# Kernel tuning notes

Measured on AMD Instinct MI355X. Metric: run time of the kernel, lower is better.

Reference implementation:

```python
import jax, jax.numpy as jnp
import numpy as np

L = 128          # lifted_dim
NS = 50000       # source nodes
NT = 50000       # target nodes
E = 640000       # edges
SLOPE = 0.01     # cfg.leaky_slope (torch LeakyReLU default)
EPS = 1e-5       # BatchNorm eps


def _glorot(key, shape):
    fan_in, fan_out = shape[0], shape[1]
    lim = np.sqrt(6.0 / (fan_in + fan_out)).astype(np.float32)
    return jax.random.uniform(key, shape, jnp.float32, -lim, lim)


def setup_inputs() -> dict:
    key = jax.random.key(0)
    ks = jax.random.split(key, 16)
    x_s = jax.random.normal(ks[0], (NS, L), jnp.float32)
    x_t = jax.random.normal(ks[1], (NT, L), jnp.float32)
    edge_index = jax.random.randint(ks[2], (2, E), 0, NT, jnp.int64)
    edge_attr = jax.random.normal(ks[3], (E, L), jnp.float32)
    x_u = jax.random.normal(ks[4], (L,), jnp.float32)
    M = 2 * L  # message_dim
    U = 4 * L  # update_dim
    params = {
        'W1': _glorot(ks[5], (M, M)), 'b1': jnp.zeros((M,), jnp.float32),
        'W2': _glorot(ks[6], (M, M)), 'b2': jnp.zeros((M,), jnp.float32),
        'U1': _glorot(ks[7], (U, U)), 'c1': jnp.zeros((U,), jnp.float32),
        'U2': _glorot(ks[8], (U, L)), 'c2': jnp.zeros((L,), jnp.float32),
        'gamma': jnp.ones((L,), jnp.float32), 'beta': jnp.zeros((L,), jnp.float32),
    }
    return dict(x_s=x_s, x_t=x_t, edge_index=edge_index, edge_attr=edge_attr, x_u=x_u, **params)


def reference(x_s, x_t, edge_index, edge_attr, x_u,
              W1, b1, W2, b2, U1, c1, U2, c2, gamma, beta):
    src, tgt = edge_index[0], edge_index[1]
    # edge messages: gather source features + edge attrs -> 2-layer MLP
    msg = jnp.concatenate([x_s[src], edge_attr], axis=1)          # [E, 2L]
    msg = jax.nn.leaky_relu(msg @ W1 + b1, negative_slope=SLOPE)
    msg = msg @ W2 + b2                                           # [E, 2L]
    # scatter-add aggregation onto target nodes
    agg = jax.ops.segment_sum(msg, tgt, num_segments=x_t.shape[0])  # [NT, 2L]
    # node update
    xu = jnp.broadcast_to(x_u[None, :], (x_t.shape[0], x_u.shape[0]))
    h = jnp.concatenate([x_t, agg, xu], axis=-1)                  # [NT, 4L]
    h = jax.nn.leaky_relu(h @ U1 + c1, negative_slope=SLOPE)
    h = h @ U2 + c2                                               # [NT, L]
    # BatchNorm1d (training mode: batch statistics, biased variance)
    mu = jnp.mean(h, axis=0)
    var = jnp.var(h, axis=0)
    return gamma * (h - mu) * jax.lax.rsqrt(var + EPS) + beta
```

## Files before the change

kernel.cpp:

```cpp
#include <hip/hip_runtime.h>

typedef unsigned int u32;
typedef unsigned short u16;
typedef __attribute__((ext_vector_type(8))) short short8;
typedef __attribute__((ext_vector_type(8))) unsigned short ushort8v;
typedef __attribute__((ext_vector_type(4))) unsigned short ushort4v;
typedef __attribute__((ext_vector_type(4))) float f32x4;

#define NSRC 50000
#define NTGT 50000
#define NEDGE 640000
#define LDIM 128
#define SLOPE 0.01f

#define MFMA(a, b, c) __builtin_amdgcn_mfma_f32_16x16x32_bf16((a), (b), (c), 0, 0, 0)

__device__ __forceinline__ u16 f2bf(float f) {
  union { float f; u32 u; } v; v.f = f;
  u32 r = v.u + 0x7FFFu + ((v.u >> 16) & 1u);
  return (u16)(r >> 16);
}
__device__ __forceinline__ float bf2f(u16 h) {
  union { u32 u; float f; } v; v.u = ((u32)h) << 16; return v.f;
}

__global__ void k_w2b(const float* __restrict__ W2, const float* __restrict__ U1,
                      float* __restrict__ w2b) {
  const int i = blockIdx.x;
  const int j = threadIdx.x;
  const float* __restrict__ u = U1 + (size_t)128 * 512;
  float a0 = 0.f, a1 = 0.f;
#pragma unroll 8
  for (int k = 0; k < 256; ++k) {
    float w = W2[(size_t)i * 256 + k];
    a0 += w * u[(size_t)k * 512 + j];
    a1 += w * u[(size_t)k * 512 + j + 256];
  }
  w2b[(size_t)i * 512 + j] = a0;
  w2b[(size_t)i * 512 + j + 256] = a1;
}

__global__ void k_bias(const float* __restrict__ U1, const float* __restrict__ xu,
                       const float* __restrict__ b2, const float* __restrict__ c1,
                       float* __restrict__ c1e, float* __restrict__ vb) {
  const int j = threadIdx.x;
  float s = c1[j];
#pragma unroll 4
  for (int k = 0; k < 128; ++k) s += xu[k] * U1[(size_t)(384 + k) * 512 + j];
  float v = 0.f;
#pragma unroll 4
  for (int k = 0; k < 256; ++k) v += b2[k] * U1[(size_t)(128 + k) * 512 + j];
  c1e[j] = s;
  vb[j] = v;
}

__global__ void k_prep(const float* __restrict__ W1, const float* __restrict__ U1,
                       const float* __restrict__ U2, const float* __restrict__ w2b,
                       u16* __restrict__ w1a, u16* __restrict__ w1b,
                       u16* __restrict__ u1e, u16* __restrict__ u2p) {
  int id = blockIdx.x * 256 + threadIdx.x;
  int lane = id & 63, quad = (lane >> 4), l16 = lane & 15;
  if (id < 4096) {
    int g = id >> 6;
    int kc = g >> 4, cb = g & 15;
    const float* s = W1 + (size_t)(kc * 32 + quad * 8) * 256 + cb * 16 + l16;
    ushort8v p;
#pragma unroll
    for (int j = 0; j < 8; ++j) p[j] = f2bf(s[(size_t)j * 256]);
    *(ushort8v*)(w1a + ((size_t)g * 64 + lane) * 8) = p;
  } else if (id < 8192) {
    int g = (id - 4096) >> 6;
    int kc = g >> 4, cb = g & 15;
    const float* s = W1 + (size_t)(128 + kc * 32 + quad * 8) * 256 + cb * 16 + l16;
    ushort8v p;
#pragma unroll
    for (int j = 0; j < 8; ++j) p[j] = f2bf(s[(size_t)j * 256]);
    *(ushort8v*)(w1b + ((size_t)g * 64 + lane) * 8) = p;
  } else if (id < 32768) {
    int g = (id - 8192) >> 6;
    int kc = g >> 5, cb = g & 31;
    int col = cb * 16 + l16;
    ushort8v p;
#pragma unroll
    for (int j = 0; j < 8; ++j) {
      int row = kc * 32 + quad * 8 + j;
      float v = (row < 128) ? U1[(size_t)row * 512 + col]
                            : w2b[(size_t)(row - 128) * 512 + col];
      p[j] = f2bf(v);
    }
    *(ushort8v*)(u1e + ((size_t)g * 64 + lane) * 8) = p;
  } else if (id < 40960) {
    int g = (id - 32768) >> 6;
    int kc = g >> 3, cb = g & 7;
    const float* s = U2 + (size_t)(kc * 32 + quad * 8) * 128 + cb * 16 + l16;
    ushort8v p;
#pragma unroll
    for (int j = 0; j < 8; ++j) p[j] = f2bf(s[(size_t)j * 128]);
    *(ushort8v*)(u2p + ((size_t)g * 64 + lane) * 8) = p;
  }
}

__global__ void k_count(const int* __restrict__ tgt, int* __restrict__ cnt,
                        int* __restrict__ rank) {
  int e = blockIdx.x * 256 + threadIdx.x;
  if (e < NEDGE) rank[e] = atomicAdd(&cnt[tgt[e]], 1);
}

__global__ void k_scan(const int* __restrict__ cnt, int* __restrict__ rowstart) {
  __shared__ int part[1024];
  int tid = threadIdx.x;
  int base = tid * 49;
  int s = 0;
  for (int i = 0; i < 49; ++i) { int idx = base + i; if (idx < NTGT) s += cnt[idx]; }
  part[tid] = s;
  __syncthreads();
  for (int off = 1; off < 1024; off <<= 1) {
    int v = (tid >= off) ? part[tid - off] : 0;
    __syncthreads();
    part[tid] += v;
    __syncthreads();
  }
  int run = (tid > 0) ? part[tid - 1] : 0;
  for (int i = 0; i < 49; ++i) {
    int idx = base + i;
    if (idx < NTGT) { rowstart[idx] = run; run += cnt[idx]; }
  }
  if (tid == 1023) rowstart[NTGT] = part[1023];
}

__global__ void k_posinv(const int* __restrict__ tgt, const int* __restrict__ rowstart,
                         const int* __restrict__ rank, int* __restrict__ order) {
  int e = blockIdx.x * 256 + threadIdx.x;
  if (e < NEDGE) order[rowstart[tgt[e]] + rank[e]] = e;
}

__global__ __launch_bounds__(256, 3) void k_pgemm(
    const float* __restrict__ xs, const u16* __restrict__ w1ap,
    const float* __restrict__ b1, u16* __restrict__ P) {
  __shared__ u16 At[64][136];
  __shared__ u16 Ot[64][264];
  const int tid = threadIdx.x;
  const int base = blockIdx.x * 64;
  {
    const int et = tid >> 2, p = tid & 3;
    const int row = base + et;
    u16* dst = &At[et][p * 32];
    if (row < NSRC) {
      const float4* f4 = (const float4*)(xs + (size_t)row * LDIM + p * 32);
#pragma unroll
      for (int i = 0; i < 4; ++i) {
        float4 a = f4[2 * i], b = f4[2 * i + 1];
        ushort8v pk = { f2bf(a.x), f2bf(a.y), f2bf(a.z), f2bf(a.w),
                        f2bf(b.x), f2bf(b.y), f2bf(b.z), f2bf(b.w) };
        *(ushort8v*)(dst + i * 8) = pk;
      }
    } else {
      ushort8v z = {0, 0, 0, 0, 0, 0, 0, 0};
#pragma unroll
      for (int i = 0; i < 4; ++i) *(ushort8v*)(dst + i * 8) = z;
    }
  }
  __syncthreads();

  const int lane = tid & 63, wid = tid >> 6;
  const int quad = lane >> 4, l16 = lane & 15;
  const int colb = wid * 64;
  const short8* __restrict__ wf = (const short8*)w1ap;

  f32x4 acc[4][4];
#pragma unroll
  for (int a = 0; a < 4; ++a)
#pragma unroll
    for (int b = 0; b < 4; ++b) acc[a][b] = (f32x4){0.f, 0.f, 0.f, 0.f};
#pragma unroll
  for (int kc = 0; kc < 4; ++kc) {
    short8 af[4], bfr[4];
#pragma unroll
    for (int ct = 0; ct < 4; ++ct)
      bfr[ct] = wf[(size_t)(kc * 16 + wid * 4 + ct) * 64 + lane];
#pragma unroll
    for (int rt = 0; rt < 4; ++rt)
      af[rt] = *(const short8*)&At[rt * 16 + l16][kc * 32 + quad * 8];
#pragma unroll
    for (int rt = 0; rt < 4; ++rt)
#pragma unroll
      for (int ct = 0; ct < 4; ++ct)
        acc[rt][ct] = MFMA(af[rt], bfr[ct], acc[rt][ct]);
  }
#pragma unroll
  for (int ct = 0; ct < 4; ++ct) {
    int col = colb + ct * 16 + l16;
    float bias = b1[col];
#pragma unroll
    for (int rt = 0; rt < 4; ++rt)
#pragma unroll
      for (int r = 0; r < 4; ++r) {
        int row = rt * 16 + quad * 4 + r;
        Ot[row][col] = f2bf(acc[rt][ct][r] + bias);
      }
  }
  __syncthreads();
  {
    const int et = tid >> 2, p = tid & 3;
    const int row = base + et;
    if (row < NSRC) {
      u16* dst = P + (size_t)row * 256 + p * 64;
      const u16* sl = &Ot[et][p * 64];
#pragma unroll
      for (int i = 0; i < 8; ++i)
        *(ushort8v*)(dst + i * 8) = *(const ushort8v*)(sl + i * 8);
    }
  }
}

__global__ __launch_bounds__(256, 4) void k_edge(
    const float* __restrict__ ea, const int* __restrict__ srcp,
    const int* __restrict__ tgtp, const int* __restrict__ order,
    const u16* __restrict__ Pg, const u16* __restrict__ w1bp,
    float* __restrict__ agg) {
  __shared__ u16 Pt[64][264];
  __shared__ int s_tgt[64];
  __shared__ unsigned long long s_mask;
  const int tid = threadIdx.x;
  const int base = blockIdx.x * 64;

  {
    const int et = tid >> 2, p = tid & 3;
    const int e = order[base + et];
    if (p == 0) s_tgt[et] = tgtp[e];
    const int sidx = srcp[e];
    const ushort8v* pr = (const ushort8v*)(Pg + (size_t)sidx * 256 + p * 64);
    u16* dst = &Pt[et][p * 64];
#pragma unroll
    for (int i = 0; i < 8; ++i) *(ushort8v*)(dst + i * 8) = pr[i];
  }
  if (tid < 64) {
    int tcur = tgtp[order[base + tid]];
    int tprv = (tid > 0) ? tgtp[order[base + tid - 1]] : tcur;
    unsigned long long m = __ballot(tcur != tprv);
    if (tid == 0) s_mask = m;
  }

  const int lane = tid & 63, wid = tid >> 6;
  const int quad = lane >> 4, l16 = lane & 15;
  const short8* __restrict__ wf = (const short8*)w1bp;

  const int myrow = wid * 16 + l16;
  const float* arow = ea + (size_t)order[base + myrow] * LDIM + quad * 8;

  short8 af[4];
#pragma unroll
  for (int kc = 0; kc < 4; ++kc) {
    f32x4 x = *(const f32x4*)(arow + kc * 32);
    f32x4 y = *(const f32x4*)(arow + kc * 32 + 4);
    af[kc] = (short8){ (short)f2bf(x[0]), (short)f2bf(x[1]),
                       (short)f2bf(x[2]), (short)f2bf(x[3]),
                       (short)f2bf(y[0]), (short)f2bf(y[1]),
                       (short)f2bf(y[2]), (short)f2bf(y[3]) };
  }

  f32x4 acc[8];
#pragma unroll
  for (int ct = 0; ct < 8; ++ct) acc[ct] = (f32x4){0.f, 0.f, 0.f, 0.f};
#pragma unroll
  for (int kc = 0; kc < 4; ++kc)
#pragma unroll
    for (int ct = 0; ct < 8; ++ct)
      acc[ct] = MFMA(af[kc], wf[(size_t)(kc * 16 + ct) * 64 + lane], acc[ct]);

  __syncthreads();

#pragma unroll
  for (int ct = 0; ct < 8; ++ct) {
    int col = ct * 16 + l16;
#pragma unroll
    for (int r = 0; r < 4; ++r) {
      int row = wid * 16 + quad * 4 + r;
      float v = acc[ct][r] + bf2f(Pt[row][col]);
      v = v > 0.f ? v : SLOPE * v;
      Pt[row][col] = f2bf(v);
    }
  }

#pragma unroll
  for (int ct = 0; ct < 8; ++ct) acc[ct] = (f32x4){0.f, 0.f, 0.f, 0.f};
#pragma unroll
  for (int kc = 0; kc < 4; ++kc)
#pragma unroll
    for (int ct = 0; ct < 8; ++ct)
      acc[ct] = MFMA(af[kc], wf[(size_t)(kc * 16 + 8 + ct) * 64 + lane], acc[ct]);

#pragma unroll
  for (int ct = 0; ct < 8; ++ct) {
    int col = 128 + ct * 16 + l16;
#pragma unroll
    for (int r = 0; r < 4; ++r) {
      int row = wid * 16 + quad * 4 + r;
      float v = acc[ct][r] + bf2f(Pt[row][col]);
      v = v > 0.f ? v : SLOPE * v;
      Pt[row][col] = f2bf(v);
    }
  }
  __syncthreads();

  {
    const unsigned long long mask = s_mask;
    const int col = tid;
    float accv = 0.f;
    int segstart = 0;
    for (int r = 0; r < 64; ++r) {
      if ((mask >> r) & 1ull) {
        float* dst = agg + (size_t)s_tgt[r - 1] * 256 + col;
        if (segstart == 0) atomicAdd(dst, accv);
        else *dst = accv;
        accv = 0.f; segstart = r;
      }
      accv += bf2f(Pt[r][col]);
    }
    atomicAdd(agg + (size_t)s_tgt[63] * 256 + col, accv);
  }
}

__global__ __launch_bounds__(256, 4) void k_node(
    const float* __restrict__ xt, const float* __restrict__ agg,
    const int* __restrict__ rowstart, const u16* __restrict__ u1e,
    const u16* __restrict__ u2p, const float* __restrict__ c1e,
    const float* __restrict__ vb, const float* __restrict__ c2,
    float* __restrict__ h2, float* __restrict__ stats) {
  __shared__ u16 ain[32][520];
  __shared__ float sdeg[32];
  const int tid = threadIdx.x;
  const int lane = tid & 63, wid = tid >> 6;
  const int quad = lane >> 4, l16 = lane & 15;
  const int tbase = blockIdx.x * 32;

  for (int s = wid; s < 32; s += 4) {
    int t = tbase + s;
    if (t < NTGT) {
      if (lane < 32) {
        float4 v = ((const float4*)(xt + (size_t)t * LDIM))[lane];
        ushort4v p = { f2bf(v.x), f2bf(v.y), f2bf(v.z), f2bf(v.w) };
        *(ushort4v*)&ain[s][lane * 4] = p;
      }
      if (lane == 0) sdeg[s] = (float)(rowstart[t + 1] - rowstart[t]);
      float4 v = ((const float4*)(agg + (size_t)t * 256))[lane];
      ushort4v p = { f2bf(v.x), f2bf(v.y), f2bf(v.z), f2bf(v.w) };
      *(ushort4v*)&ain[s][128 + lane * 4] = p;
    } else {
      ushort8v z = {0, 0, 0, 0, 0, 0, 0, 0};
      *(ushort8v*)&ain[s][lane * 8] = z;
      if (lane == 0) sdeg[s] = 0.f;
    }
  }
  __syncthreads();

  const short8* __restrict__ u1f = (const short8*)u1e;
  const short8* __restrict__ u2f = (const short8*)u2p;

  f32x4 acc[2][2][4];
#pragma unroll
  for (int h = 0; h < 2; ++h)
#pragma unroll
    for (int a = 0; a < 2; ++a)
#pragma unroll
      for (int b = 0; b < 4; ++b) acc[h][a][b] = (f32x4){0.f, 0.f, 0.f, 0.f};

#pragma unroll 2
  for (int kc = 0; kc < 12; ++kc) {
    short8 af[2];
#pragma unroll
    for (int rt = 0; rt < 2; ++rt)
      af[rt] = *(const short8*)&ain[rt * 16 + l16][kc * 32 + quad * 8];
#pragma unroll
    for (int h = 0; h < 2; ++h) {
      short8 bfr[4];
#pragma unroll
      for (int ct = 0; ct < 4; ++ct)
        bfr[ct] = u1f[(size_t)(kc * 32 + h * 16 + wid * 4 + ct) * 64 + lane];
#pragma unroll
      for (int rt = 0; rt < 2; ++rt)
#pragma unroll
        for (int ct = 0; ct < 4; ++ct)
          acc[h][rt][ct] = MFMA(af[rt], bfr[ct], acc[h][rt][ct]);
    }
  }
  __syncthreads();
#pragma unroll
  for (int h = 0; h < 2; ++h)
#pragma unroll
    for (int ct = 0; ct < 4; ++ct) {
      int col = h * 256 + wid * 64 + ct * 16 + l16;
      float cb = c1e[col], vbb = vb[col];
#pragma unroll
      for (int rt = 0; rt < 2; ++rt)
#pragma unroll
        for (int r = 0; r < 4; ++r) {
          int row = rt * 16 + quad * 4 + r;
          float v = acc[h][rt][ct][r] + cb + sdeg[row] * vbb;
          v = v > 0.f ? v : SLOPE * v;
          ain[row][col] = f2bf(v);
        }
    }
  __syncthreads();

  const int colb2 = wid * 32;
  f32x4 acc2[2][2];
#pragma unroll
  for (int a = 0; a < 2; ++a)
#pragma unroll
    for (int b = 0; b < 2; ++b) acc2[a][b] = (f32x4){0.f, 0.f, 0.f, 0.f};
#pragma unroll 4
  for (int kc = 0; kc < 16; ++kc) {
    short8 af[2], bfr[2];
#pragma unroll
    for (int ct = 0; ct < 2; ++ct)
      bfr[ct] = u2f[(size_t)(kc * 8 + wid * 2 + ct) * 64 + lane];
#pragma unroll
    for (int rt = 0; rt < 2; ++rt)
      af[rt] = *(const short8*)&ain[rt * 16 + l16][kc * 32 + quad * 8];
#pragma unroll
    for (int rt = 0; rt < 2; ++rt)
#pragma unroll
      for (int ct = 0; ct < 2; ++ct)
        acc2[rt][ct] = MFMA(af[rt], bfr[ct], acc2[rt][ct]);
  }
  float s1[2] = {0.f, 0.f}, s2[2] = {0.f, 0.f};
#pragma unroll
  for (int ct = 0; ct < 2; ++ct) {
    int col = colb2 + ct * 16 + l16;
    float cb = c2[col];
#pragma unroll
    for (int rt = 0; rt < 2; ++rt)
#pragma unroll
      for (int r = 0; r < 4; ++r) {
        int row = rt * 16 + quad * 4 + r;
        int t = tbase + row;
        if (t < NTGT) {
          float v = acc2[rt][ct][r] + cb;
          h2[(size_t)t * LDIM + col] = v;
          s1[ct] += v; s2[ct] += v * v;
        }
      }
  }
#pragma unroll
  for (int ct = 0; ct < 2; ++ct) {
    float a = s1[ct], b = s2[ct];
    a += __shfl_down(a, 32); b += __shfl_down(b, 32);
    a += __shfl_down(a, 16); b += __shfl_down(b, 16);
    if (lane < 16) {
      atomicAdd(&stats[colb2 + ct * 16 + l16], a);
      atomicAdd(&stats[128 + colb2 + ct * 16 + l16], b);
    }
  }
}

__global__ void k_bnfin(const float* __restrict__ stats, const float* __restrict__ gamma,
                        const float* __restrict__ beta, float* __restrict__ ss) {
  int c = threadIdx.x;
  if (c < 128) {
    float mu = stats[c] * (1.0f / NTGT);
    float var = stats[128 + c] * (1.0f / NTGT) - mu * mu;
    float rs = rsqrtf(var + 1e-5f);
    float sc = gamma[c] * rs;
    ss[c] = sc;
    ss[128 + c] = beta[c] - mu * sc;
  }
}

__global__ void k_bnapply(const float* __restrict__ h2, const float* __restrict__ ss,
                          float* __restrict__ out) {
  int i = blockIdx.x * 256 + threadIdx.x;
  const int total = NTGT * LDIM / 4;
  const float4* h4 = (const float4*)h2;
  const float4* sc4 = (const float4*)ss;
  const float4* sh4 = (const float4*)(ss + 128);
  float4* o4 = (float4*)out;
  for (; i < total; i += gridDim.x * 256) {
    int cg = i & 31;
    float4 h = h4[i], sc = sc4[cg], sh = sh4[cg];
    float4 r = { h.x * sc.x + sh.x, h.y * sc.y + sh.y,
                 h.z * sc.z + sh.z, h.w * sc.w + sh.w };
    o4[i] = r;
  }
}

extern "C" void kernel_launch(void* const* d_in, const int* in_sizes, int n_in,
                              void* d_out, int out_size, void* d_ws, size_t ws_size,
                              hipStream_t stream) {
  (void)in_sizes; (void)n_in; (void)out_size; (void)ws_size;
  const float* xs    = (const float*)d_in[0];
  const float* xt    = (const float*)d_in[1];
  const int*   ei    = (const int*)d_in[2];
  const float* ea    = (const float*)d_in[3];
  const float* xu    = (const float*)d_in[4];
  const float* W1    = (const float*)d_in[5];
  const float* b1    = (const float*)d_in[6];
  const float* W2    = (const float*)d_in[7];
  const float* b2    = (const float*)d_in[8];
  const float* U1    = (const float*)d_in[9];
  const float* c1    = (const float*)d_in[10];
  const float* U2    = (const float*)d_in[11];
  const float* c2    = (const float*)d_in[12];
  const float* gamma = (const float*)d_in[13];
  const float* beta  = (const float*)d_in[14];

  char* ws = (char*)d_ws;
  u16* w1a   = (u16*)(ws + 0x000000);
  u16* w1b   = (u16*)(ws + 0x010000);
  u16* u1e   = (u16*)(ws + 0x020000);
  u16* u2p   = (u16*)(ws + 0x080000);
  float* w2b = (float*)(ws + 0x0A0000);
  float* c1e = (float*)(ws + 0x120000);
  float* vbv = (float*)(ws + 0x120800);
  int* cnt   = (int*)(ws + 0x130000);
  int* rowst = (int*)(ws + 0x161000);
  int* rank  = (int*)(ws + 0x192000);
  float* stats = (float*)(ws + 0x404000);
  float* ss    = stats + 256;
  int* order = (int*)(ws + 0x405000);
  float* agg = (float*)(ws + 0x680000);
  u16*   Pbuf = (u16*)(ws + 0x3760000);
  float* h2   = (float*)(ws + 0x3760000);

  const int* srcp = ei;
  const int* tgtp = ei + NEDGE;

  hipMemsetAsync(cnt, 0, NTGT * 4, stream);
  hipMemsetAsync(stats, 0, 256 * 4, stream);
  hipMemsetAsync(agg, 0, (size_t)NTGT * 256 * 4, stream);
  k_w2b<<<256, 256, 0, stream>>>(W2, U1, w2b);
  k_bias<<<1, 512, 0, stream>>>(U1, xu, b2, c1, c1e, vbv);
  k_prep<<<160, 256, 0, stream>>>(W1, U1, U2, w2b, w1a, w1b, u1e, u2p);
  k_count<<<2500, 256, 0, stream>>>(tgtp, cnt, rank);
  k_scan<<<1, 1024, 0, stream>>>(cnt, rowst);
  k_posinv<<<2500, 256, 0, stream>>>(tgtp, rowst, rank, order);
  k_pgemm<<<782, 256, 0, stream>>>(xs, w1a, b1, Pbuf);
  k_edge<<<10000, 256, 0, stream>>>(ea, srcp, tgtp, order, Pbuf, w1b, agg);
  k_node<<<1563, 256, 0, stream>>>(xt, agg, rowst, u1e, u2p, c1e, vbv, c2, h2, stats);
  k_bnfin<<<1, 128, 0, stream>>>(stats, gamma, beta, ss);
  k_bnapply<<<6250, 256, 0, stream>>>(h2, ss, (float*)d_out);
}
```

Before: 948.6 us.

## Process two edge tiles per block and prefetch next tile's edge attributes

The edge kernel now handles two 64-edge tiles per block in a loop, halving the grid. While the first tile computes, it issues the global loads of edge_attr rows for the second tile into registers, hiding that load latency. The segmented reduction also batches 16 LDS reads at a time before the branchy accumulate loop. This costs extra registers for the prefetch buffer, which may reduce occupancy, and fewer blocks means less parallelism to hide latency.

```diff
diff --git a/kernel.cpp b/kernel.cpp
--- a/kernel.cpp
+++ b/kernel.cpp
@@ -222,102 +222,132 @@
   __shared__ int s_tgt[64];
   __shared__ unsigned long long s_mask;
   const int tid = threadIdx.x;
-  const int base = blockIdx.x * 64;
-
-  {
-    const int et = tid >> 2, p = tid & 3;
-    const int e = order[base + et];
-    if (p == 0) s_tgt[et] = tgtp[e];
-    const int sidx = srcp[e];
-    const ushort8v* pr = (const ushort8v*)(Pg + (size_t)sidx * 256 + p * 64);
-    u16* dst = &Pt[et][p * 64];
-#pragma unroll
-    for (int i = 0; i < 8; ++i) *(ushort8v*)(dst + i * 8) = pr[i];
-  }
-  if (tid < 64) {
-    int tcur = tgtp[order[base + tid]];
-    int tprv = (tid > 0) ? tgtp[order[base + tid - 1]] : tcur;
-    unsigned long long m = __ballot(tcur != tprv);
-    if (tid == 0) s_mask = m;
-  }
-
   const int lane = tid & 63, wid = tid >> 6;
   const int quad = lane >> 4, l16 = lane & 15;
+  const int myrow = wid * 16 + l16;
+  const int base0 = blockIdx.x * 128;
   const short8* __restrict__ wf = (const short8*)w1bp;
 
-  const int myrow = wid * 16 + l16;
-  const float* arow = ea + (size_t)order[base + myrow] * LDIM + quad * 8;
-
-  short8 af[4];
-#pragma unroll
-  for (int kc = 0; kc < 4; ++kc) {
-    f32x4 x = *(const f32x4*)(arow + kc * 32);
-    f32x4 y = *(const f32x4*)(arow + kc * 32 + 4);
-    af[kc] = (short8){ (short)f2bf(x[0]), (short)f2bf(x[1]),
-                       (short)f2bf(x[2]), (short)f2bf(x[3]),
-                       (short)f2bf(y[0]), (short)f2bf(y[1]),
-                       (short)f2bf(y[2]), (short)f2bf(y[3]) };
-  }
-
-  f32x4 acc[8];
-#pragma unroll
-  for (int ct = 0; ct < 8; ++ct) acc[ct] = (f32x4){0.f, 0.f, 0.f, 0.f};
-#pragma unroll
-  for (int kc = 0; kc < 4; ++kc)
-#pragma unroll
-    for (int ct = 0; ct < 8; ++ct)
-      acc[ct] = MFMA(af[kc], wf[(size_t)(kc * 16 + ct) * 64 + lane], acc[ct]);
-
-  __syncthreads();
-
-#pragma unroll
-  for (int ct = 0; ct < 8; ++ct) {
-    int col = ct * 16 + l16;
-#pragma unroll
-    for (int r = 0; r < 4; ++r) {
-      int row = wid * 16 + quad * 4 + r;
-      float v = acc[ct][r] + bf2f(Pt[row][col]);
-      v = v > 0.f ? v : SLOPE * v;
-      Pt[row][col] = f2bf(v);
-    }
-  }
-
-#pragma unroll
-  for (int ct = 0; ct < 8; ++ct) acc[ct] = (f32x4){0.f, 0.f, 0.f, 0.f};
-#pragma unroll
-  for (int kc = 0; kc < 4; ++kc)
-#pragma unroll
-    for (int ct = 0; ct < 8; ++ct)
-      acc[ct] = MFMA(af[kc], wf[(size_t)(kc * 16 + 8 + ct) * 64 + lane], acc[ct]);
-
-#pragma unroll
-  for (int ct = 0; ct < 8; ++ct) {
-    int col = 128 + ct * 16 + l16;
-#pragma unroll
-    for (int r = 0; r < 4; ++r) {
-      int row = wid * 16 + quad * 4 + r;
-      float v = acc[ct][r] + bf2f(Pt[row][col]);
-      v = v > 0.f ? v : SLOPE * v;
-      Pt[row][col] = f2bf(v);
-    }
-  }
-  __syncthreads();
-
+  const int em0 = order[base0 + myrow];
+  const int em1 = order[base0 + 64 + myrow];
+  f32x4 a0[8];
   {
-    const unsigned long long mask = s_mask;
-    const int col = tid;
-    float accv = 0.f;
-    int segstart = 0;
-    for (int r = 0; r < 64; ++r) {
-      if ((mask >> r) & 1ull) {
-        float* dst = agg + (size_t)s_tgt[r - 1] * 256 + col;
-        if (segstart == 0) atomicAdd(dst, accv);
-        else *dst = accv;
-        accv = 0.f; segstart = r;
-      }
-      accv += bf2f(Pt[r][col]);
-    }
-    atomicAdd(agg + (size_t)s_tgt[63] * 256 + col, accv);
+    const float* ar = ea + (size_t)em0 * LDIM + quad * 8;
+#pragma unroll
+    for (int kc = 0; kc < 4; ++kc) {
+      a0[2 * kc]     = *(const f32x4*)(ar + kc * 32);
+      a0[2 * kc + 1] = *(const f32x4*)(ar + kc * 32 + 4);
+    }
+  }
+
+#pragma unroll 1
+  for (int it = 0; it < 2; ++it) {
+    const int base = base0 + it * 64;
+
+    {
+      const int et = tid >> 2, p = tid & 3;
+      const int e = order[base + et];
+      if (p == 0) s_tgt[et] = tgtp[e];
+      const int sidx = srcp[e];
+      const ushort8v* pr = (const ushort8v*)(Pg + (size_t)sidx * 256 + p * 64);
+      u16* dst = &Pt[et][p * 64];
+#pragma unroll
+      for (int i = 0; i < 8; ++i) *(ushort8v*)(dst + i * 8) = pr[i];
+    }
+    if (tid < 64) {
+      int tcur = tgtp[order[base + tid]];
+      int tprv = (tid > 0) ? tgtp[order[base + tid - 1]] : tcur;
+      unsigned long long m = __ballot(tcur != tprv);
+      if (tid == 0) s_mask = m;
+    }
+
+    short8 af[4];
+#pragma unroll
+    for (int kc = 0; kc < 4; ++kc) {
+      f32x4 x = a0[2 * kc], y = a0[2 * kc + 1];
+      af[kc] = (short8){ (short)f2bf(x[0]), (short)f2bf(x[1]),
+                         (short)f2bf(x[2]), (short)f2bf(x[3]),
+                         (short)f2bf(y[0]), (short)f2bf(y[1]),
+                         (short)f2bf(y[2]), (short)f2bf(y[3]) };
+    }
+    if (it == 0) {
+      const float* ar = ea + (size_t)em1 * LDIM + quad * 8;
+#pragma unroll
+      for (int kc = 0; kc < 4; ++kc) {
+        a0[2 * kc]     = *(const f32x4*)(ar + kc * 32);
+        a0[2 * kc + 1] = *(const f32x4*)(ar + kc * 32 + 4);
+      }
+    }
+
+    f32x4 acc[8];
+#pragma unroll
+    for (int ct = 0; ct < 8; ++ct) acc[ct] = (f32x4){0.f, 0.f, 0.f, 0.f};
+#pragma unroll
+    for (int kc = 0; kc < 4; ++kc)
+#pragma unroll
+      for (int ct = 0; ct < 8; ++ct)
+        acc[ct] = MFMA(af[kc], wf[(size_t)(kc * 16 + ct) * 64 + lane], acc[ct]);
+
+    __syncthreads();
+
+#pragma unroll
+    for (int ct = 0; ct < 8; ++ct) {
+      int col = ct * 16 + l16;
+#pragma unroll
+      for (int r = 0; r < 4; ++r) {
+        int row = wid * 16 + quad * 4 + r;
+        float v = acc[ct][r] + bf2f(Pt[row][col]);
+        v = v > 0.f ? v : SLOPE * v;
+        Pt[row][col] = f2bf(v);
+      }
+    }
+
+#pragma unroll
+    for (int ct = 0; ct < 8; ++ct) acc[ct] = (f32x4){0.f, 0.f, 0.f, 0.f};
+#pragma unroll
+    for (int kc = 0; kc < 4; ++kc)
+#pragma unroll
+      for (int ct = 0; ct < 8; ++ct)
+        acc[ct] = MFMA(af[kc], wf[(size_t)(kc * 16 + 8 + ct) * 64 + lane], acc[ct]);
+
+#pragma unroll
+    for (int ct = 0; ct < 8; ++ct) {
+      int col = 128 + ct * 16 + l16;
+#pragma unroll
+      for (int r = 0; r < 4; ++r) {
+        int row = wid * 16 + quad * 4 + r;
+        float v = acc[ct][r] + bf2f(Pt[row][col]);
+        v = v > 0.f ? v : SLOPE * v;
+        Pt[row][col] = f2bf(v);
+      }
+    }
+    __syncthreads();
+
+    {
+      const unsigned long long mask = s_mask;
+      const int col = tid;
+      float accv = 0.f;
+      int segstart = 0;
+#pragma unroll
+      for (int rb = 0; rb < 4; ++rb) {
+        float v[16];
+#pragma unroll
+        for (int j = 0; j < 16; ++j) v[j] = bf2f(Pt[rb * 16 + j][col]);
+#pragma unroll
+        for (int j = 0; j < 16; ++j) {
+          int r = rb * 16 + j;
+          if ((mask >> r) & 1ull) {
+            float* dst = agg + (size_t)s_tgt[r - 1] * 256 + col;
+            if (segstart == 0) atomicAdd(dst, accv);
+            else *dst = accv;
+            accv = 0.f; segstart = r;
+          }
+          accv += v[j];
+        }
+      }
+      atomicAdd(agg + (size_t)s_tgt[63] * 256 + col, accv);
+    }
+    if (it == 0) __syncthreads();
   }
 }
 
@@ -535,7 +565,7 @@
   k_scan<<<1, 1024, 0, stream>>>(cnt, rowst);
   k_posinv<<<2500, 256, 0, stream>>>(tgtp, rowst, rank, order);
   k_pgemm<<<782, 256, 0, stream>>>(xs, w1a, b1, Pbuf);
-  k_edge<<<10000, 256, 0, stream>>>(ea, srcp, tgtp, order, Pbuf, w1b, agg);
+  k_edge<<<5000, 256, 0, stream>>>(ea, srcp, tgtp, order, Pbuf, w1b, agg);
   k_node<<<1563, 256, 0, stream>>>(xt, agg, rowst, u1e, u2p, c1e, vbv, c2, h2, stats);
   k_bnfin<<<1, 128, 0, stream>>>(stats, gamma, beta, ss);
   k_bnapply<<<6250, 256, 0, stream>>>(h2, ss, (float*)d_out);
```

Measured after the change: 1.682 ms. 77.3% more time.
